# Kernel tuning notes

Measured on AMD Instinct MI355X. Metric: run time of the kernel, lower is better.

The kernel has to match this reference:

```python
import jax, jax.numpy as jnp
import numpy as np

EPS = 1e-5
HEADS, DQK, DV, SD = 1, 12, 12, 2  # heads, dim_qk, dim_v, spatial_down


def group_norm(x, w, b):
    # GroupNorm(1, C): normalize over all non-batch dims, per-channel affine
    axes = tuple(range(1, x.ndim))
    m = x.mean(axis=axes, keepdims=True)
    v = x.var(axis=axes, keepdims=True)
    xn = (x - m) * jax.lax.rsqrt(v + EPS)
    shp = (1, -1) + (1,) * (x.ndim - 2)
    return xn * w.reshape(shp) + b.reshape(shp)


def setup_inputs() -> dict:
    key = jax.random.key(0)
    ks = jax.random.split(key, 6)
    B, Ccv, D, H, W = 4, 32, 48, 64, 128
    Cf, Hs, Ws = 256, 8, 16  # Hs*Ws = 128 == max_tokens -> token_pool is identity
    cost = jax.random.normal(ks[0], (B, Ccv, D, H, W), jnp.float32)
    feat_s4 = jax.random.normal(ks[1], (B, Cf, Hs, Ws), jnp.float32)
    E = HEADS * DQK
    w_q = jax.random.normal(ks[2], (E, Ccv), jnp.float32) * (1.0 / np.sqrt(Ccv))
    w_k = jax.random.normal(ks[3], (E, Cf), jnp.float32) * (1.0 / np.sqrt(Cf))
    w_v = jax.random.normal(ks[4], (HEADS * DV, Cf), jnp.float32) * (1.0 / np.sqrt(Cf))
    w_out = jax.random.normal(ks[5], (Ccv, HEADS * DV), jnp.float32) * (1.0 / np.sqrt(HEADS * DV))
    return {
        'cost': cost, 'feat_s4': feat_s4,
        'w_q': w_q, 'w_k': w_k, 'w_v': w_v, 'w_out': w_out,
        'gn_in_w': jnp.ones((Ccv,), jnp.float32), 'gn_in_b': jnp.zeros((Ccv,), jnp.float32),
        'gn_out_w': jnp.ones((Ccv,), jnp.float32), 'gn_out_b': jnp.zeros((Ccv,), jnp.float32),
        'gamma': jnp.float32(0.1),
    }


def reference(cost, feat_s4, w_q, w_k, w_v, w_out, gn_in_w, gn_in_b, gn_out_w, gn_out_b, gamma):
    B, Ccv, D, H, W = cost.shape
    x_in = group_norm(cost, gn_in_w, gn_in_b)
    # avg_pool3d kernel/stride (1, SD, SD)
    Hq, Wq = H // SD, W // SD
    xq = x_in.reshape(B, Ccv, D, Hq, SD, Wq, SD).mean(axis=(4, 6))
    # 1x1 conv projections == channel matmuls
    q = jnp.einsum('bcdhw,ec->bedhw', xq, w_q)          # (B, h*dqk, D, Hq, Wq)
    k = jnp.einsum('bchw,ec->behw', feat_s4, w_k)       # (B, h*dqk, Hs, Ws)
    v = jnp.einsum('bchw,ec->behw', feat_s4, w_v)       # (B, h*dv, Hs, Ws)
    Ns = k.shape[2] * k.shape[3]
    kf = k.reshape(B, HEADS, DQK, Ns)                   # (B, h, dqk, Ns)
    vf = v.reshape(B, HEADS, DV, Ns)                    # (B, h, dv, Ns)
    N = D * Hq * Wq
    qf = q.reshape(B, HEADS, DQK, N).transpose(0, 1, 3, 2)  # (B, h, N, dqk)
    logits = jnp.einsum('bhnq,bhqs->bhns', qf, kf) * (DQK ** -0.5)
    attn = jax.nn.softmax(logits, axis=-1)
    out = jnp.einsum('bhns,bhds->bhnd', attn, vf)       # (B, h, N, dv)
    out = out.transpose(0, 1, 3, 2).reshape(B, HEADS * DV, D, Hq, Wq)
    out = jnp.einsum('bedhw,ce->bcdhw', out, w_out)     # (B, Ccv, D, Hq, Wq)
    # trilinear upsample (align_corners=False == half-pixel, jax.image default)
    out = jax.image.resize(out, (B, Ccv, D, H, W), method='trilinear')
    out = out.astype(jnp.bfloat16).astype(jnp.float32)  # replicate torch bf16 cast
    return group_norm(cost + gamma * out, gn_out_w, gn_out_b)
```

## Files before the change

kernel.cpp:

```cpp
#include <hip/hip_runtime.h>
#include <hip/hip_fp16.h>

typedef float f4v __attribute__((ext_vector_type(4)));

namespace {
constexpr int Bn = 4, Cn = 32, Dn = 48, Hn = 64, Wn = 128;
constexpr int HQ = 32, WQ = 64;
constexpr int NPB = Dn * HQ * WQ;
constexpr int DHW = Dn * Hn * Wn;
constexpr int PERB = Cn * DHW;
constexpr int NS = 128, En = 12;
constexpr float EPS = 1e-5f;
constexpr float SQK = 0.2886751345948129f;
constexpr int NB1 = 192;

constexpr size_t OFF_ZB  = 0;
constexpr size_t OFF_QR  = 6291456;
constexpr size_t OFF_P1  = OFF_QR + 2359296;
constexpr size_t OFF_P2  = OFF_P1 + 1536;
constexpr size_t OFF_PKV = OFF_P2 + 12288;
constexpr size_t OFF_CB  = OFF_PKV + 49152;
constexpr size_t WS_NEED_FLOATS = OFF_CB + 25165824;
}

__device__ inline unsigned short bf16b(float x) {
    unsigned u = __float_as_uint(x);
    return (unsigned short)((u + 0x7fffu + ((u >> 16) & 1u)) >> 16);
}
__device__ inline float b2f(unsigned short h) { return __uint_as_float(((unsigned)h) << 16); }
__device__ inline float bf16_rne(float x) {
    unsigned u = __float_as_uint(x);
    u = (u + 0x7fffu + ((u >> 16) & 1u)) & 0xffff0000u;
    return __uint_as_float(u);
}

__device__ inline float2 block_red2(float s, float ss) {
#pragma unroll
    for (int off = 32; off; off >>= 1) {
        s += __shfl_down(s, off, 64);
        ss += __shfl_down(ss, off, 64);
    }
    __shared__ float red[8];
    int lane = threadIdx.x & 63, w = threadIdx.x >> 6;
    __syncthreads();
    if (!lane) { red[w] = s; red[4 + w] = ss; }
    __syncthreads();
    return make_float2(red[0] + red[1] + red[2] + red[3],
                       red[4] + red[5] + red[6] + red[7]);
}

template <bool CB>
__global__ __launch_bounds__(256) void k1_pool(const float* __restrict__ cost,
                                               const float* __restrict__ feat,
                                               const float* __restrict__ w_q,
                                               const float* __restrict__ w_k,
                                               const float* __restrict__ w_v,
                                               const float* __restrict__ gniw,
                                               unsigned short* __restrict__ qr,
                                               float2* __restrict__ part1,
                                               float* __restrict__ pkv,
                                               __half* __restrict__ cb) {
    __shared__ float wqg[En * Cn];
    const int b = blockIdx.y, tid = threadIdx.x;
    for (int i = tid; i < En * Cn; i += 256) wqg[i] = w_q[i] * gniw[i & 31];
    __syncthreads();
    const int np = blockIdx.x * 512 + tid * 2;
    const int d = np >> 11, r = np & 2047, hq = r >> 6, wq = r & 63;
    const size_t fbase = (size_t)b * PERB + (size_t)d * 8192 + (size_t)(hq * 2) * Wn + wq * 2;
    float s = 0.f, ss = 0.f;
    float q0[En], q1[En];
#pragma unroll
    for (int e = 0; e < En; ++e) { q0[e] = 0.f; q1[e] = 0.f; }
#pragma unroll 4
    for (int c = 0; c < Cn; ++c) {
        const size_t off = fbase + (size_t)c * DHW;
        f4v t0, t1;
        if (CB) {
            t0 = __builtin_nontemporal_load((const f4v*)(cost + off));
            t1 = __builtin_nontemporal_load((const f4v*)(cost + off + Wn));
            __half2 h01 = __halves2half2(__float2half_rn(t0.x), __float2half_rn(t0.y));
            __half2 h23 = __halves2half2(__float2half_rn(t0.z), __float2half_rn(t0.w));
            __half2 g01 = __halves2half2(__float2half_rn(t1.x), __float2half_rn(t1.y));
            __half2 g23 = __halves2half2(__float2half_rn(t1.z), __float2half_rn(t1.w));
            uint2 pk0 = make_uint2(*(unsigned*)&h01, *(unsigned*)&h23);
            uint2 pk1 = make_uint2(*(unsigned*)&g01, *(unsigned*)&g23);
            *reinterpret_cast<uint2*>(cb + off) = pk0;
            *reinterpret_cast<uint2*>(cb + off + Wn) = pk1;
        } else {
            t0 = *reinterpret_cast<const f4v*>(cost + off);
            t1 = *reinterpret_cast<const f4v*>(cost + off + Wn);
        }
        float p0 = t0.x + t0.y + t1.x + t1.y;
        float p1 = t0.z + t0.w + t1.z + t1.w;
        s += p0 + p1;
        ss += t0.x * t0.x + t0.y * t0.y + t0.z * t0.z + t0.w * t0.w +
              t1.x * t1.x + t1.y * t1.y + t1.z * t1.z + t1.w * t1.w;
        p0 *= 0.25f; p1 *= 0.25f;
#pragma unroll
        for (int e = 0; e < En; ++e) {
            q0[e] += wqg[e * Cn + c] * p0;
            q1[e] += wqg[e * Cn + c] * p1;
        }
    }
#pragma unroll
    for (int e = 0; e < En; ++e) {
        unsigned pk = (unsigned)bf16b(q0[e]) | ((unsigned)bf16b(q1[e]) << 16);
        *reinterpret_cast<unsigned*>(qr + (size_t)(b * En + e) * NPB + np) = pk;
    }
    float2 rp = block_red2(s, ss);
    if (!tid) part1[b * NB1 + blockIdx.x] = rp;

    if (b == 0 && blockIdx.x < 16 && tid < NS) {
        const int g = blockIdx.x, kb = g >> 2, cg = g & 3, sI = tid;
        float kk[En], vv[En];
#pragma unroll
        for (int e = 0; e < En; ++e) { kk[e] = 0.f; vv[e] = 0.f; }
        for (int ch = 0; ch < 4; ++ch) {
            const int c0 = cg * 64 + ch * 16;
            float f[16];
#pragma unroll
            for (int jj = 0; jj < 16; ++jj) f[jj] = feat[(size_t)(kb * 256 + c0 + jj) * NS + sI];
#pragma unroll
            for (int jj = 0; jj < 16; ++jj) {
                const int c = c0 + jj;
#pragma unroll
                for (int e = 0; e < En; ++e) {
                    kk[e] += w_k[e * 256 + c] * f[jj];
                    vv[e] += w_v[e * 256 + c] * f[jj];
                }
            }
        }
#pragma unroll
        for (int e = 0; e < En; ++e) {
            pkv[((size_t)(g * NS + sI)) * 24 + e] = kk[e];
            pkv[((size_t)(g * NS + sI)) * 24 + 12 + e] = vv[e];
        }
    }
}

__global__ __launch_bounds__(256) void k_attn(const unsigned short* __restrict__ qr,
                                              const float* __restrict__ pkv,
                                              const float* __restrict__ w_q,
                                              const float* __restrict__ gniw,
                                              const float* __restrict__ gnib,
                                              const float2* __restrict__ part1,
                                              const float* __restrict__ w_out,
                                              unsigned short* __restrict__ zb) {
    __shared__ float Ks[NS * En], Vs[NS * En], WOs[Cn * En], QBs[En];
    __shared__ float kred[2], kscs_sh;
    const int x = blockIdx.x, b = blockIdx.y, tid = threadIdx.x;

    float sP = 0.f, ssP = 0.f;
    if (tid < NB1) {
        float2 v = part1[b * NB1 + tid];
        sP = v.x; ssP = v.y;
    }
    float2 tP = block_red2(sP, ssP);
    const float mGN = tP.x / (float)PERB;
    const float rsGN = rsqrtf(tP.y / (float)PERB - mGN * mGN + EPS);

    for (int i = tid; i < NS * En; i += 256) {
        int s = i / En, e = i - s * En;
        size_t base = ((size_t)((b * 4) * NS + s)) * 24 + e;
        Ks[i] = pkv[base] + pkv[base + 3072] + pkv[base + 6144] + pkv[base + 9216];
        Vs[i] = pkv[base + 12] + pkv[base + 3084] + pkv[base + 6156] + pkv[base + 9228];
    }
    for (int i = tid; i < Cn * En; i += 256) WOs[i] = w_out[i];
    if (tid < En) {
        float acc = 0.f;
        for (int c = 0; c < Cn; ++c)
            acc += w_q[tid * Cn + c] * (gnib[c] - mGN * rsGN * gniw[c]);
        QBs[tid] = SQK * acc;
    }
    __syncthreads();
    if (tid < NS) {
        float n2 = 0.f;
#pragma unroll
        for (int e = 0; e < En; ++e) { float k = Ks[tid * En + e]; n2 += k * k; }
#pragma unroll
        for (int off = 32; off; off >>= 1) n2 = fmaxf(n2, __shfl_down(n2, off, 64));
        if (!(tid & 63)) kred[tid >> 6] = n2;
    }
    __syncthreads();
    if (!tid) kscs_sh = sqrtf(fmaxf(kred[0], kred[1]));
    __syncthreads();
    const float kscs = kscs_sh;
    const float qsc = rsGN * SQK;

    const int nbase = x * 768 + tid;

    f4v q[3][3];
    float ub[3];
#pragma unroll
    for (int p = 0; p < 3; ++p) {
        const int n = nbase + 256 * p;
        float qn2 = 0.f;
#pragma unroll
        for (int v = 0; v < 3; ++v) {
            f4v t;
#pragma unroll
            for (int u = 0; u < 4; ++u) {
                int e = v * 4 + u;
                float qe = qsc * b2f(qr[(size_t)(b * En + e) * NPB + n]) + QBs[e];
                t[u] = qe;
                qn2 += qe * qe;
            }
            q[p][v] = t;
        }
        ub[p] = sqrtf(qn2) * kscs;
    }

    f4v o0[3], o1[3], o2[3];
    float l[3];
#pragma unroll
    for (int p = 0; p < 3; ++p) {
        o0[p] = (f4v)(0.f); o1[p] = (f4v)(0.f); o2[p] = (f4v)(0.f);
        l[p] = 0.f;
    }
    const f4v* K4 = (const f4v*)Ks;
    const f4v* V4 = (const f4v*)Vs;
    for (int s = 0; s < NS; ++s) {
        f4v k0 = K4[s * 3], k1 = K4[s * 3 + 1], k2 = K4[s * 3 + 2];
        f4v v0 = V4[s * 3], v1 = V4[s * 3 + 1], v2 = V4[s * 3 + 2];
#pragma unroll
        for (int p = 0; p < 3; ++p) {
            f4v d4 = q[p][0] * k0 + q[p][1] * k1 + q[p][2] * k2;
            float dot = (d4.x + d4.y) + (d4.z + d4.w);
            float pe = __expf(dot - ub[p]);
            l[p] += pe;
            o0[p] += pe * v0; o1[p] += pe * v1; o2[p] += pe * v2;
        }
    }

    const f4v* WO4 = (const f4v*)WOs;
#pragma unroll
    for (int p = 0; p < 3; ++p) {
        const float inv = 1.0f / l[p];
        const int n = nbase + 256 * p;
        for (int c = 0; c < Cn; ++c) {
            f4v z4 = WO4[c * 3] * o0[p] + WO4[c * 3 + 1] * o1[p] + WO4[c * 3 + 2] * o2[p];
            float z = ((z4.x + z4.y) + (z4.z + z4.w)) * inv;
            zb[(size_t)(b * Cn + c) * NPB + n] = bf16b(z);
        }
    }
}

__device__ inline void up_quad(int qd, const unsigned short* __restrict__ zs,
                               float g, float (&u4)[4]) {
    int h = qd >> 5, w4 = (qd & 31) << 2;
    int h0 = (h - 1) >> 1;
    float wh0 = (h & 1) ? 0.75f : 0.25f;
    int h1 = h0 + 1;
    h0 = h0 < 0 ? 0 : h0; h1 = h1 > HQ - 1 ? HQ - 1 : h1;
    const unsigned short* r0 = zs + h0 * WQ;
    const unsigned short* r1 = zs + h1 * WQ;
#pragma unroll
    for (int p = 0; p < 4; ++p) {
        int w = w4 + p;
        int w0 = (w - 1) >> 1;
        float ww0 = (w & 1) ? 0.75f : 0.25f;
        int w1 = w0 + 1;
        w0 = w0 < 0 ? 0 : w0; w1 = w1 > WQ - 1 ? WQ - 1 : w1;
        float u = wh0 * (ww0 * b2f(r0[w0]) + (1.f - ww0) * b2f(r0[w1])) +
                  (1.f - wh0) * (ww0 * b2f(r1[w0]) + (1.f - ww0) * b2f(r1[w1]));
        u4[p] = g * bf16_rne(u);
    }
}

template <bool CB>
__global__ __launch_bounds__(256) void k_ystats(const float* __restrict__ cost,
                                                const __half* __restrict__ cb,
                                                const unsigned short* __restrict__ zb,
                                                const float* __restrict__ gamma_p,
                                                float2* __restrict__ part2) {
    const int blk = blockIdx.x;
    __shared__ unsigned short zs[HQ * WQ];
    const int tid = threadIdx.x;
    {
        const unsigned int* zsrc = (const unsigned int*)(zb + (size_t)blk * 2048);
        for (int i = tid; i < 1024; i += 256) ((unsigned int*)zs)[i] = zsrc[i];
    }
    __syncthreads();
    const float g = gamma_p[0];
    float s = 0.f, ss = 0.f;
#pragma unroll
    for (int k = 0; k < 8; ++k) {
        int qd = tid + 256 * k;
        float u4[4];
        up_quad(qd, zs, g, u4);
        float cvv[4];
        if (CB) {
            uint2 pk = *reinterpret_cast<const uint2*>(cb + (size_t)blk * 8192 + qd * 4);
            float2 f01 = __half22float2(*reinterpret_cast<__half2*>(&pk.x));
            float2 f23 = __half22float2(*reinterpret_cast<__half2*>(&pk.y));
            cvv[0] = f01.x; cvv[1] = f01.y; cvv[2] = f23.x; cvv[3] = f23.y;
        } else {
            f4v cv = ((const f4v*)(cost + (size_t)blk * 8192))[qd];
            cvv[0] = cv.x; cvv[1] = cv.y; cvv[2] = cv.z; cvv[3] = cv.w;
        }
#pragma unroll
        for (int p = 0; p < 4; ++p) {
            float y = cvv[p] + u4[p];
            s += y; ss += y * y;
        }
    }
    float2 rp = block_red2(s, ss);
    if (!tid) part2[blk] = rp;
}

template <bool CB>
__global__ __launch_bounds__(256) void k_final(const float* __restrict__ cost,
                                               const __half* __restrict__ cb,
                                               const unsigned short* __restrict__ zb,
                                               const float* __restrict__ gamma_p,
                                               const float2* __restrict__ part2,
                                               const float* __restrict__ gow,
                                               const float* __restrict__ gob,
                                               float* __restrict__ out) {
    const int blk = blockIdx.x;
    const int b = blk / (Cn * Dn);
    const int c = (blk / Dn) % Cn;
    const int tid = threadIdx.x;

    float sP = 0.f, ssP = 0.f;
    for (int i = tid; i < Cn * Dn; i += 256) {
        float2 v = part2[b * Cn * Dn + i];
        sP += v.x; ssP += v.y;
    }
    float2 tP = block_red2(sP, ssP);
    const float m = tP.x / (float)PERB;
    const float rs = rsqrtf(tP.y / (float)PERB - m * m + EPS);

    __shared__ unsigned short zs[HQ * WQ];
    {
        const unsigned int* zsrc = (const unsigned int*)(zb + (size_t)blk * 2048);
        for (int i = tid; i < 1024; i += 256) ((unsigned int*)zs)[i] = zsrc[i];
    }
    __syncthreads();
    const float g = gamma_p[0];
    const float sc = rs * gow[c], bi = gob[c];
    f4v* oq = (f4v*)(out + (size_t)blk * 8192);
#pragma unroll
    for (int k = 0; k < 8; ++k) {
        int qd = tid + 256 * k;
        float u4[4];
        up_quad(qd, zs, g, u4);
        float cvv[4];
        if (CB) {
            uint2 pk = *reinterpret_cast<const uint2*>(cb + (size_t)blk * 8192 + qd * 4);
            float2 f01 = __half22float2(*reinterpret_cast<__half2*>(&pk.x));
            float2 f23 = __half22float2(*reinterpret_cast<__half2*>(&pk.y));
            cvv[0] = f01.x; cvv[1] = f01.y; cvv[2] = f23.x; cvv[3] = f23.y;
        } else {
            f4v cv = ((const f4v*)(cost + (size_t)blk * 8192))[qd];
            cvv[0] = cv.x; cvv[1] = cv.y; cvv[2] = cv.z; cvv[3] = cv.w;
        }
        f4v ov;
#pragma unroll
        for (int p = 0; p < 4; ++p) {
            float y = cvv[p] + u4[p];
            ov[p] = (y - m) * sc + bi;
        }
        __builtin_nontemporal_store(ov, oq + qd);
    }
}

extern "C" void kernel_launch(void* const* d_in, const int* in_sizes, int n_in,
                              void* d_out, int out_size, void* d_ws, size_t ws_size,
                              hipStream_t stream) {
    const float* cost  = (const float*)d_in[0];
    const float* feat  = (const float*)d_in[1];
    const float* w_q   = (const float*)d_in[2];
    const float* w_k   = (const float*)d_in[3];
    const float* w_v   = (const float*)d_in[4];
    const float* w_out = (const float*)d_in[5];
    const float* gniw  = (const float*)d_in[6];
    const float* gnib  = (const float*)d_in[7];
    const float* gow   = (const float*)d_in[8];
    const float* gob   = (const float*)d_in[9];
    const float* gamma = (const float*)d_in[10];

    float* ws = (float*)d_ws;
    float* outp = (float*)d_out;

    unsigned short* zb = (unsigned short*)(ws + OFF_ZB);
    unsigned short* qr = (unsigned short*)(ws + OFF_QR);
    float2* part1 = (float2*)(ws + OFF_P1);
    float2* part2 = (float2*)(ws + OFF_P2);
    float* pkv = ws + OFF_PKV;
    __half* cb = (__half*)(ws + OFF_CB);

    const bool useCB = ws_size >= WS_NEED_FLOATS * sizeof(float);

    if (useCB) {
        k1_pool<true><<<dim3(NB1, Bn), 256, 0, stream>>>(cost, feat, w_q, w_k, w_v, gniw,
                                                         qr, part1, pkv, cb);
        k_attn<<<dim3(128, Bn), 256, 0, stream>>>(qr, pkv, w_q, gniw, gnib, part1, w_out, zb);
        k_ystats<true><<<Bn * Cn * Dn, 256, 0, stream>>>(cost, cb, zb, gamma, part2);
        k_final<true><<<Bn * Cn * Dn, 256, 0, stream>>>(cost, cb, zb, gamma, part2, gow, gob, outp);
    } else {
        k1_pool<false><<<dim3(NB1, Bn), 256, 0, stream>>>(cost, feat, w_q, w_k, w_v, gniw,
                                                          qr, part1, pkv, cb);
        k_attn<<<dim3(128, Bn), 256, 0, stream>>>(qr, pkv, w_q, gniw, gnib, part1, w_out, zb);
        k_ystats<false><<<Bn * Cn * Dn, 256, 0, stream>>>(cost, cb, zb, gamma, part2);
        k_final<false><<<Bn * Cn * Dn, 256, 0, stream>>>(cost, cb, zb, gamma, part2, gow, gob, outp);
    }
}
```

Baseline: 193.0 us.

## Derive output GroupNorm stats analytically, dropping the ystats pass and fp16 cost copy

The separate k_ystats pass, which re-read the cost volume to get the sum and sum-of-squares of cost+gamma*upsample, is removed. Those statistics are now built algebraically from three sources: the input stats, cross terms between the pooled cost (written as a bf16 buffer) and the low-res attention output z, and a closed-form weighted sum of z products for the trilinear upsample's squared energy. All of these are computed inside the attention kernel. The fp16 copy of cost is dropped, so k_final reads the fp32 cost again. This saves a full pass over the cost volume, at the cost of an extra bf16 pooled buffer, more work and barriers in k_attn, and possible precision loss in the derived variance.

```diff
diff --git a/kernel.cpp b/kernel.cpp
--- a/kernel.cpp
+++ b/kernel.cpp
@@ -1,5 +1,4 @@
 #include <hip/hip_runtime.h>
-#include <hip/hip_fp16.h>
 
 typedef float f4v __attribute__((ext_vector_type(4)));
 
@@ -13,14 +12,14 @@
 constexpr float EPS = 1e-5f;
 constexpr float SQK = 0.2886751345948129f;
 constexpr int NB1 = 192;
+constexpr int NBA = 128;
 
 constexpr size_t OFF_ZB  = 0;
-constexpr size_t OFF_QR  = 6291456;
+constexpr size_t OFF_PB  = 6291456;
+constexpr size_t OFF_QR  = OFF_PB + 6291456;
 constexpr size_t OFF_P1  = OFF_QR + 2359296;
 constexpr size_t OFF_P2  = OFF_P1 + 1536;
-constexpr size_t OFF_PKV = OFF_P2 + 12288;
-constexpr size_t OFF_CB  = OFF_PKV + 49152;
-constexpr size_t WS_NEED_FLOATS = OFF_CB + 25165824;
+constexpr size_t OFF_PKV = OFF_P2 + 2048;
 }
 
 __device__ inline unsigned short bf16b(float x) {
@@ -49,7 +48,6 @@
                        red[4] + red[5] + red[6] + red[7]);
 }
 
-template <bool CB>
 __global__ __launch_bounds__(256) void k1_pool(const float* __restrict__ cost,
                                                const float* __restrict__ feat,
                                                const float* __restrict__ w_q,
@@ -57,9 +55,9 @@
                                                const float* __restrict__ w_v,
                                                const float* __restrict__ gniw,
                                                unsigned short* __restrict__ qr,
+                                               unsigned short* __restrict__ pb,
                                                float2* __restrict__ part1,
-                                               float* __restrict__ pkv,
-                                               __half* __restrict__ cb) {
+                                               float* __restrict__ pkv) {
     __shared__ float wqg[En * Cn];
     const int b = blockIdx.y, tid = threadIdx.x;
     for (int i = tid; i < En * Cn; i += 256) wqg[i] = w_q[i] * gniw[i & 31];
@@ -74,28 +72,16 @@
 #pragma unroll 4
     for (int c = 0; c < Cn; ++c) {
         const size_t off = fbase + (size_t)c * DHW;
-        f4v t0, t1;
-        if (CB) {
-            t0 = __builtin_nontemporal_load((const f4v*)(cost + off));
-            t1 = __builtin_nontemporal_load((const f4v*)(cost + off + Wn));
-            __half2 h01 = __halves2half2(__float2half_rn(t0.x), __float2half_rn(t0.y));
-            __half2 h23 = __halves2half2(__float2half_rn(t0.z), __float2half_rn(t0.w));
-            __half2 g01 = __halves2half2(__float2half_rn(t1.x), __float2half_rn(t1.y));
-            __half2 g23 = __halves2half2(__float2half_rn(t1.z), __float2half_rn(t1.w));
-            uint2 pk0 = make_uint2(*(unsigned*)&h01, *(unsigned*)&h23);
-            uint2 pk1 = make_uint2(*(unsigned*)&g01, *(unsigned*)&g23);
-            *reinterpret_cast<uint2*>(cb + off) = pk0;
-            *reinterpret_cast<uint2*>(cb + off + Wn) = pk1;
-        } else {
-            t0 = *reinterpret_cast<const f4v*>(cost + off);
-            t1 = *reinterpret_cast<const f4v*>(cost + off + Wn);
-        }
-        float p0 = t0.x + t0.y + t1.x + t1.y;
-        float p1 = t0.z + t0.w + t1.z + t1.w;
-        s += p0 + p1;
+        f4v t0 = *reinterpret_cast<const f4v*>(cost + off);
+        f4v t1 = *reinterpret_cast<const f4v*>(cost + off + Wn);
+        float ps0 = t0.x + t0.y + t1.x + t1.y;
+        float ps1 = t0.z + t0.w + t1.z + t1.w;
+        s += ps0 + ps1;
         ss += t0.x * t0.x + t0.y * t0.y + t0.z * t0.z + t0.w * t0.w +
               t1.x * t1.x + t1.y * t1.y + t1.z * t1.z + t1.w * t1.w;
-        p0 *= 0.25f; p1 *= 0.25f;
+        float p0 = 0.25f * ps0, p1 = 0.25f * ps1;
+        unsigned pk = (unsigned)bf16b(p0) | ((unsigned)bf16b(p1) << 16);
+        *reinterpret_cast<unsigned*>(pb + (size_t)(b * Cn + c) * NPB + np) = pk;
 #pragma unroll
         for (int e = 0; e < En; ++e) {
             q0[e] += wqg[e * Cn + c] * p0;
@@ -139,14 +125,17 @@
 }
 
 __global__ __launch_bounds__(256) void k_attn(const unsigned short* __restrict__ qr,
+                                              const unsigned short* __restrict__ pb,
                                               const float* __restrict__ pkv,
                                               const float* __restrict__ w_q,
                                               const float* __restrict__ gniw,
                                               const float* __restrict__ gnib,
                                               const float2* __restrict__ part1,
                                               const float* __restrict__ w_out,
-                                              unsigned short* __restrict__ zb) {
+                                              unsigned short* __restrict__ zb,
+                                              float4* __restrict__ part2) {
     __shared__ float Ks[NS * En], Vs[NS * En], WOs[Cn * En], QBs[En];
+    __shared__ float zrowf[768];
     __shared__ float kred[2], kscs_sh;
     const int x = blockIdx.x, b = blockIdx.y, tid = threadIdx.x;
 
@@ -231,18 +220,53 @@
             o0[p] += pe * v0; o1[p] += pe * v1; o2[p] += pe * v2;
         }
     }
+    float invl[3];
+#pragma unroll
+    for (int p = 0; p < 3; ++p) invl[p] = 1.0f / l[p];
 
     const f4v* WO4 = (const f4v*)WOs;
-#pragma unroll
-    for (int p = 0; p < 3; ++p) {
-        const float inv = 1.0f / l[p];
-        const int n = nbase + 256 * p;
-        for (int c = 0; c < Cn; ++c) {
+    float sz = 0.f, spz = 0.f, t2 = 0.f;
+    for (int c = 0; c < Cn; ++c) {
+        float zr[3];
+#pragma unroll
+        for (int p = 0; p < 3; ++p) {
             f4v z4 = WO4[c * 3] * o0[p] + WO4[c * 3 + 1] * o1[p] + WO4[c * 3 + 2] * o2[p];
-            float z = ((z4.x + z4.y) + (z4.z + z4.w)) * inv;
-            zb[(size_t)(b * Cn + c) * NPB + n] = bf16b(z);
-        }
-    }
+            float z = ((z4.x + z4.y) + (z4.z + z4.w)) * invl[p];
+            unsigned short zv = bf16b(z);
+            zb[(size_t)(b * Cn + c) * NPB + nbase + 256 * p] = zv;
+            float zf = b2f(zv);
+            zrowf[tid + 256 * p] = zf;
+            zr[p] = zf;
+        }
+        __syncthreads();
+#pragma unroll
+        for (int p = 0; p < 3; ++p) {
+            const int lidx = tid + 256 * p;
+            const int n = x * 768 + lidx;
+            const int w = n & 63, h = (n >> 6) & 31;
+            const float z = zr[p];
+            const float Dh = (h == 0 || h == 31) ? 1.625f : 1.25f;
+            const float Dw = (w == 0 || w == 63) ? 1.625f : 1.25f;
+            float acc = Dh * Dw * z * z;
+            const bool okw = (w < 63);
+            const bool okh = (h < 31) && (lidx < 704);
+            float zw = okw ? zrowf[lidx + 1] : 0.f;
+            float zh = okh ? zrowf[lidx + 64] : 0.f;
+            acc += 0.75f * Dh * z * zw;
+            acc += 0.75f * Dw * z * zh;
+            if (okw && okh) {
+                float zd = zrowf[lidx + 65];
+                acc += 0.28125f * (z * zd + zw * zh);
+            }
+            t2 += acc;
+            sz += z;
+            spz += z * b2f(pb[(size_t)(b * Cn + c) * NPB + n]);
+        }
+        __syncthreads();
+    }
+    float2 rA = block_red2(sz, spz);
+    float2 rB = block_red2(t2, 0.f);
+    if (!tid) part2[b * NBA + x] = make_float4(rA.x, rA.y, rB.x, 0.f);
 }
 
 __device__ inline void up_quad(int qd, const unsigned short* __restrict__ zs,
@@ -267,53 +291,11 @@
     }
 }
 
-template <bool CB>
-__global__ __launch_bounds__(256) void k_ystats(const float* __restrict__ cost,
-                                                const __half* __restrict__ cb,
-                                                const unsigned short* __restrict__ zb,
-                                                const float* __restrict__ gamma_p,
-                                                float2* __restrict__ part2) {
-    const int blk = blockIdx.x;
-    __shared__ unsigned short zs[HQ * WQ];
-    const int tid = threadIdx.x;
-    {
-        const unsigned int* zsrc = (const unsigned int*)(zb + (size_t)blk * 2048);
-        for (int i = tid; i < 1024; i += 256) ((unsigned int*)zs)[i] = zsrc[i];
-    }
-    __syncthreads();
-    const float g = gamma_p[0];
-    float s = 0.f, ss = 0.f;
-#pragma unroll
-    for (int k = 0; k < 8; ++k) {
-        int qd = tid + 256 * k;
-        float u4[4];
-        up_quad(qd, zs, g, u4);
-        float cvv[4];
-        if (CB) {
-            uint2 pk = *reinterpret_cast<const uint2*>(cb + (size_t)blk * 8192 + qd * 4);
-            float2 f01 = __half22float2(*reinterpret_cast<__half2*>(&pk.x));
-            float2 f23 = __half22float2(*reinterpret_cast<__half2*>(&pk.y));
-            cvv[0] = f01.x; cvv[1] = f01.y; cvv[2] = f23.x; cvv[3] = f23.y;
-        } else {
-            f4v cv = ((const f4v*)(cost + (size_t)blk * 8192))[qd];
-            cvv[0] = cv.x; cvv[1] = cv.y; cvv[2] = cv.z; cvv[3] = cv.w;
-        }
-#pragma unroll
-        for (int p = 0; p < 4; ++p) {
-            float y = cvv[p] + u4[p];
-            s += y; ss += y * y;
-        }
-    }
-    float2 rp = block_red2(s, ss);
-    if (!tid) part2[blk] = rp;
-}
-
-template <bool CB>
 __global__ __launch_bounds__(256) void k_final(const float* __restrict__ cost,
-                                               const __half* __restrict__ cb,
                                                const unsigned short* __restrict__ zb,
                                                const float* __restrict__ gamma_p,
-                                               const float2* __restrict__ part2,
+                                               const float2* __restrict__ part1,
+                                               const float4* __restrict__ part2,
                                                const float* __restrict__ gow,
                                                const float* __restrict__ gob,
                                                float* __restrict__ out) {
@@ -321,15 +303,26 @@
     const int b = blk / (Cn * Dn);
     const int c = (blk / Dn) % Cn;
     const int tid = threadIdx.x;
-
-    float sP = 0.f, ssP = 0.f;
-    for (int i = tid; i < Cn * Dn; i += 256) {
-        float2 v = part2[b * Cn * Dn + i];
-        sP += v.x; ssP += v.y;
-    }
-    float2 tP = block_red2(sP, ssP);
-    const float m = tP.x / (float)PERB;
-    const float rs = rsqrtf(tP.y / (float)PERB - m * m + EPS);
+    const float g = gamma_p[0];
+
+    float sc_ = 0.f, scc = 0.f;
+    if (tid < NB1) {
+        float2 v = part1[b * NB1 + tid];
+        sc_ = v.x; scc = v.y;
+    }
+    float2 tA = block_red2(sc_, scc);
+    float sz = 0.f, spz = 0.f, t2 = 0.f;
+    if (tid < NBA) {
+        float4 v = part2[b * NBA + tid];
+        sz = v.x; spz = v.y; t2 = v.z;
+    }
+    float2 tB = block_red2(sz, spz);
+    float2 tC = block_red2(t2, 0.f);
+    const float Sy = tA.x + 4.f * g * tB.x;
+    const float Syy = tA.y + 8.f * g * tB.y + g * g * tC.x;
+    const float m = Sy / (float)PERB;
+    const float var = Syy / (float)PERB - m * m;
+    const float rs = rsqrtf(var + EPS);
 
     __shared__ unsigned short zs[HQ * WQ];
     {
@@ -337,30 +330,20 @@
         for (int i = tid; i < 1024; i += 256) ((unsigned int*)zs)[i] = zsrc[i];
     }
     __syncthreads();
-    const float g = gamma_p[0];
     const float sc = rs * gow[c], bi = gob[c];
+    const f4v* cq = (const f4v*)(cost + (size_t)blk * 8192);
     f4v* oq = (f4v*)(out + (size_t)blk * 8192);
 #pragma unroll
     for (int k = 0; k < 8; ++k) {
         int qd = tid + 256 * k;
         float u4[4];
         up_quad(qd, zs, g, u4);
-        float cvv[4];
-        if (CB) {
-            uint2 pk = *reinterpret_cast<const uint2*>(cb + (size_t)blk * 8192 + qd * 4);
-            float2 f01 = __half22float2(*reinterpret_cast<__half2*>(&pk.x));
-            float2 f23 = __half22float2(*reinterpret_cast<__half2*>(&pk.y));
-            cvv[0] = f01.x; cvv[1] = f01.y; cvv[2] = f23.x; cvv[3] = f23.y;
-        } else {
-            f4v cv = ((const f4v*)(cost + (size_t)blk * 8192))[qd];
-            cvv[0] = cv.x; cvv[1] = cv.y; cvv[2] = cv.z; cvv[3] = cv.w;
-        }
+        f4v cv = cq[qd];
         f4v ov;
-#pragma unroll
-        for (int p = 0; p < 4; ++p) {
-            float y = cvv[p] + u4[p];
-            ov[p] = (y - m) * sc + bi;
-        }
+        ov.x = (cv.x + u4[0] - m) * sc + bi;
+        ov.y = (cv.y + u4[1] - m) * sc + bi;
+        ov.z = (cv.z + u4[2] - m) * sc + bi;
+        ov.w = (cv.w + u4[3] - m) * sc + bi;
         __builtin_nontemporal_store(ov, oq + qd);
     }
 }
@@ -384,25 +367,15 @@
     float* outp = (float*)d_out;
 
     unsigned short* zb = (unsigned short*)(ws + OFF_ZB);
+    unsigned short* pb = (unsigned short*)(ws + OFF_PB);
     unsigned short* qr = (unsigned short*)(ws + OFF_QR);
     float2* part1 = (float2*)(ws + OFF_P1);
-    float2* part2 = (float2*)(ws + OFF_P2);
+    float4* part2 = (float4*)(ws + OFF_P2);
     float* pkv = ws + OFF_PKV;
-    __half* cb = (__half*)(ws + OFF_CB);
-
-    const bool useCB = ws_size >= WS_NEED_FLOATS * sizeof(float);
-
-    if (useCB) {
-        k1_pool<true><<<dim3(NB1, Bn), 256, 0, stream>>>(cost, feat, w_q, w_k, w_v, gniw,
-                                                         qr, part1, pkv, cb);
-        k_attn<<<dim3(128, Bn), 256, 0, stream>>>(qr, pkv, w_q, gniw, gnib, part1, w_out, zb);
-        k_ystats<true><<<Bn * Cn * Dn, 256, 0, stream>>>(cost, cb, zb, gamma, part2);
-        k_final<true><<<Bn * Cn * Dn, 256, 0, stream>>>(cost, cb, zb, gamma, part2, gow, gob, outp);
-    } else {
-        k1_pool<false><<<dim3(NB1, Bn), 256, 0, stream>>>(cost, feat, w_q, w_k, w_v, gniw,
-                                                          qr, part1, pkv, cb);
-        k_attn<<<dim3(128, Bn), 256, 0, stream>>>(qr, pkv, w_q, gniw, gnib, part1, w_out, zb);
-        k_ystats<false><<<Bn * Cn * Dn, 256, 0, stream>>>(cost, cb, zb, gamma, part2);
-        k_final<false><<<Bn * Cn * Dn, 256, 0, stream>>>(cost, cb, zb, gamma, part2, gow, gob, outp);
-    }
-}
+
+    k1_pool<<<dim3(NB1, Bn), 256, 0, stream>>>(cost, feat, w_q, w_k, w_v, gniw,
+                                               qr, pb, part1, pkv);
+    k_attn<<<dim3(NBA, Bn), 256, 0, stream>>>(qr, pb, pkv, w_q, gniw, gnib, part1,
+                                              w_out, zb, part2);
+    k_final<<<Bn * Cn * Dn, 256, 0, stream>>>(cost, zb, gamma, part1, part2, gow, gob, outp);
+}
```

Result: slower. 211.3 us (+9.5%).
